# Optimization experiments

Measured on AMD Instinct MI355X. Metric: run time of the kernel, lower is better.

The kernel has to match this reference:

```python
import jax, jax.numpy as jnp
import numpy as np
import math

B, T, C, H = 2, 2048, 1024, 16
HD = C // H

def setup_inputs() -> dict:
    key = jax.random.key(0)
    ks = jax.random.split(key, 5)
    s_in = 1.0 / math.sqrt(C)
    x = jax.random.normal(ks[0], (B, T, C), dtype=jnp.float32)
    W_attn = jax.random.normal(ks[1], (C, 3 * C), dtype=jnp.float32) * s_in
    b_attn = jnp.zeros((3 * C,), dtype=jnp.float32)
    W_proj = jax.random.normal(ks[2], (C, C), dtype=jnp.float32) * s_in
    b_proj = jnp.zeros((C,), dtype=jnp.float32)
    return {"x": x, "W_attn": W_attn, "b_attn": b_attn, "W_proj": W_proj, "b_proj": b_proj}

def reference(x, W_attn, b_attn, W_proj, b_proj):
    Bx, Tx, Cx = x.shape
    c = x @ W_attn + b_attn  # [B,T,3C]
    q, k, v = jnp.split(c, 3, axis=2)
    # [B,T,H,hd] -> [B,H,T,hd]
    q = q.reshape(Bx, Tx, H, HD).transpose(0, 2, 1, 3)
    k = k.reshape(Bx, Tx, H, HD).transpose(0, 2, 1, 3)
    v = v.reshape(Bx, Tx, H, HD).transpose(0, 2, 1, 3)
    # NOTE: module scales by 1/sqrt(C), not 1/sqrt(head_dim)
    attn = jnp.einsum('bhqd,bhkd->bhqk', q, k) * (1.0 / math.sqrt(Cx))
    causal = jnp.tril(jnp.ones((Tx, Tx), dtype=bool))
    attn = jnp.where(causal[None, None], attn, -jnp.inf)
    attn = jax.nn.softmax(attn, axis=-1)
    y = jnp.einsum('bhqk,bhkd->bhqd', attn, v)
    y = y.transpose(0, 2, 1, 3).reshape(Bx, Tx, Cx)
    return y @ W_proj + b_proj
```

## Files before the change

### kernel.cpp

```cpp
#include <hip/hip_runtime.h>
#include <math.h>

#define Bv 2
#define Tv 2048
#define Cv 1024
#define Hv 16
#define HDv 64
#define Mv (Bv * Tv)
#define SZv (Bv * Hv * Tv * HDv)

typedef short bf16x8 __attribute__((ext_vector_type(8)));
typedef float f32x4 __attribute__((ext_vector_type(4)));

static __device__ __forceinline__ unsigned short f2bf(float f) {
    unsigned u = __float_as_uint(f);
    u += 0x7fffu + ((u >> 16) & 1u);
    return (unsigned short)(u >> 16);
}

static __device__ __forceinline__ unsigned f2bf2(float a, float b) {
    unsigned r;
    asm("v_cvt_pk_bf16_f32 %0, %1, %2" : "=v"(r) : "v"(a), "v"(b));
    return r;
}

#define AS1 __attribute__((address_space(1)))
#define AS3 __attribute__((address_space(3)))
#define GLD16(gp, lp) __builtin_amdgcn_global_load_lds( \
    (AS1 const void*)(const void*)(gp), (AS3 void*)(void*)(lp), 16, 0, 0)

#define WAITVM(n) asm volatile("s_waitcnt vmcnt(" #n ")" ::: "memory")
#define WAITLGKM0 asm volatile("s_waitcnt lgkmcnt(0)" ::: "memory")
#define BARRIER   asm volatile("s_barrier" ::: "memory")

__global__ __launch_bounds__(256) void prep_kernel(
    const float* __restrict__ x, const float* __restrict__ Wa,
    const float* __restrict__ Wp,
    unsigned short* __restrict__ xB, unsigned short* __restrict__ WaT,
    unsigned short* __restrict__ WpT)
{
    __shared__ float tile[32][33];
    const int bid = blockIdx.x;
    const int tid = threadIdx.x;

    if (bid < 4096) {
        int i = bid * 256 + tid;
        float4 f = ((const float4*)x)[i];
        ushort4 u;
        u.x = f2bf(f.x); u.y = f2bf(f.y); u.z = f2bf(f.z); u.w = f2bf(f.w);
        ((ushort4*)xB)[i] = u;
        return;
    }
    const float* src; unsigned short* dst; int Ncols, bi;
    if (bid < 7168) { bi = bid - 4096; Ncols = 3072; src = Wa; dst = WaT; }
    else            { bi = bid - 7168; Ncols = 1024; src = Wp; dst = WpT; }
    const int nct = Ncols / 32;
    const int c0 = (bi % nct) * 32, r0 = (bi / nct) * 32;
    const int tx = tid & 31, ty = tid >> 5;
    #pragma unroll
    for (int i = 0; i < 4; ++i)
        tile[ty + i * 8][tx] = src[(size_t)(r0 + ty + i * 8) * Ncols + c0 + tx];
    __syncthreads();
    #pragma unroll
    for (int i = 0; i < 4; ++i)
        dst[(size_t)(c0 + ty + i * 8) * Cv + r0 + tx] = f2bf(tile[tx][ty + i * 8]);
}

template<int AG>
__device__ __forceinline__ void mm_mainloop_1024(
    const unsigned short* __restrict__ A, const unsigned short* __restrict__ Bt,
    unsigned short* lds, int rowBase, int colBase, f32x4 acc[][4])
{
    const int tid  = threadIdx.x;
    const int lane = tid & 63;
    const int w    = tid >> 6;
    const int quad = lane >> 4, l15 = lane & 15;
    const int wm = (w >> 1) * (32 * AG), wn = (w & 1) * 64;
    const int K = 1024;
    constexpr int ASZ = 2048 * AG;
    constexpr int BUF = ASZ + 4096;
    constexpr int MI  = 2 * AG;

    size_t offA[AG]; unsigned short* ldsA[AG];
    size_t offB[2];  unsigned short* ldsB[2];
    #pragma unroll
    for (int i = 0; i < AG; ++i) {
        int g = w * (64 * AG) + i * 64 + lane;
        int r = g >> 2, kc = (g & 3) ^ ((r >> 1) & 3);
        offA[i] = (size_t)(rowBase + r) * K + kc * 8;
        ldsA[i] = lds + (w * AG + i) * 512;
    }
    #pragma unroll
    for (int i = 0; i < 2; ++i) {
        int g = w * 128 + i * 64 + lane;
        int r = g >> 2, kc = (g & 3) ^ ((r >> 1) & 3);
        offB[i] = (size_t)(colBase + r) * K + kc * 8;
        ldsB[i] = lds + ASZ + (w * 2 + i) * 512;
    }

    const int sw = quad ^ ((l15 >> 1) & 3);
    int aoff[MI], boff[4];
    #pragma unroll
    for (int i = 0; i < MI; ++i) aoff[i] = ((wm + i * 16 + l15) * 4 + sw) * 8;
    #pragma unroll
    for (int i = 0; i < 4; ++i)  boff[i] = ASZ + ((wn + i * 16 + l15) * 4 + sw) * 8;

    #pragma unroll
    for (int t = 0; t < 2; ++t) {
        #pragma unroll
        for (int i = 0; i < AG; ++i) GLD16(A + offA[i] + t * 32, ldsA[i] + t * BUF);
        #pragma unroll
        for (int i = 0; i < 2; ++i)  GLD16(Bt + offB[i] + t * 32, ldsB[i] + t * BUF);
    }

    int cur = 0;
    for (int i = 0; i < 32; ++i) {
        if (i < 31) {
            if constexpr (AG == 2) { WAITVM(4); } else { WAITVM(3); }
        } else { WAITVM(0); }
        BARRIER;
        if (i < 30) {
            int nb = cur + 2 * BUF; if (nb >= 3 * BUF) nb -= 3 * BUF;
            const int k2 = (i + 2) * 32;
            #pragma unroll
            for (int ai = 0; ai < AG; ++ai) GLD16(A + offA[ai] + k2, ldsA[ai] + nb);
            #pragma unroll
            for (int bi = 0; bi < 2; ++bi)  GLD16(Bt + offB[bi] + k2, ldsB[bi] + nb);
        }

        bf16x8 a[MI], b[4];
        #pragma unroll
        for (int j = 0; j < MI; ++j) a[j] = *(const bf16x8*)(lds + cur + aoff[j]);
        #pragma unroll
        for (int j = 0; j < 4; ++j)  b[j] = *(const bf16x8*)(lds + cur + boff[j]);

        #pragma unroll
        for (int mi = 0; mi < MI; ++mi)
            #pragma unroll
            for (int ni = 0; ni < 4; ++ni)
                acc[mi][ni] = __builtin_amdgcn_mfma_f32_16x16x32_bf16(
                    a[mi], b[ni], acc[mi][ni], 0, 0, 0);

        cur += BUF; if (cur == 3 * BUF) cur = 0;
    }
}

__global__ __launch_bounds__(256) void qkv_mm_kernel(
    const unsigned short* __restrict__ xB, const unsigned short* __restrict__ WaT,
    const float* __restrict__ bias,
    unsigned short* __restrict__ qB, unsigned short* __restrict__ kB,
    unsigned short* __restrict__ vT)
{
    __shared__ __align__(16) unsigned short lds[24576];
    const int rowBase = blockIdx.y * 128;
    const int colBase = blockIdx.x * 128;

    f32x4 acc[4][4];
    #pragma unroll
    for (int i = 0; i < 4; ++i)
        #pragma unroll
        for (int j = 0; j < 4; ++j) acc[i][j] = (f32x4){0.f, 0.f, 0.f, 0.f};

    mm_mainloop_1024<2>(xB, WaT, lds, rowBase, colBase, acc);
    __syncthreads();

    const int tid = threadIdx.x, lane = tid & 63, w = tid >> 6;
    const int quad = lane >> 4, l15 = lane & 15;
    const int wm = (w >> 1) * 64, wn = (w & 1) * 64;
    const int s = colBase / Cv;
    const int tloc = rowBase & (Tv - 1);
    const int bh0 = (rowBase / Tv) * Hv + (colBase % Cv) / HDv;

    if (s < 2) {
        const float qs = (s == 0) ? 0.04508422f : 1.0f;
        #pragma unroll
        for (int mi = 0; mi < 4; ++mi)
            #pragma unroll
            for (int ni = 0; ni < 4; ++ni) {
                float bv = bias[colBase + wn + ni * 16 + l15];
                #pragma unroll
                for (int r = 0; r < 4; ++r) {
                    int m = wm + mi * 16 + quad * 4 + r;
                    int n = wn + ni * 16 + l15;
                    lds[m * 136 + n] = f2bf((acc[mi][ni][r] + bv) * qs);
                }
            }
        __syncthreads();
        unsigned short* dst = (s == 0) ? qB : kB;
        #pragma unroll
        for (int it = 0; it < 8; ++it) {
            int cc = tid + it * 256;
            int m = cc >> 4, j = cc & 15;
            uint4 v = *(const uint4*)(lds + m * 136 + j * 8);
            int hh = j >> 3, d0 = (j & 7) * 8;
            *(uint4*)(dst + ((size_t)(bh0 + hh) * Tv + tloc + m) * HDv + d0) = v;
        }
    } else {
        #pragma unroll
        for (int mi = 0; mi < 4; ++mi)
            #pragma unroll
            for (int ni = 0; ni < 4; ++ni) {
                float bv = bias[colBase + wn + ni * 16 + l15];
                #pragma unroll
                for (int r = 0; r < 4; ++r) {
                    int m = wm + mi * 16 + quad * 4 + r;
                    int n = wn + ni * 16 + l15;
                    lds[n * 136 + m] = f2bf(acc[mi][ni][r] + bv);
                }
            }
        __syncthreads();
        #pragma unroll
        for (int it = 0; it < 8; ++it) {
            int cc = tid + it * 256;
            int n = cc >> 4, j = cc & 15;
            uint4 v = *(const uint4*)(lds + n * 136 + j * 8);
            int hh = n >> 6, d = n & 63;
            *(uint4*)(vT + ((size_t)(bh0 + hh) * HDv + d) * Tv + tloc + j * 8) = v;
        }
    }
}

__global__ __launch_bounds__(256) void proj_mm_kernel(
    const unsigned short* __restrict__ y0B, const unsigned short* __restrict__ WpT,
    const float* __restrict__ bias, float* __restrict__ out)
{
    __shared__ __align__(16) unsigned short lds[18432];
    const int rowBase = blockIdx.y * 64;
    const int colBase = blockIdx.x * 128;

    f32x4 acc[2][4];
    #pragma unroll
    for (int i = 0; i < 2; ++i)
        #pragma unroll
        for (int j = 0; j < 4; ++j) acc[i][j] = (f32x4){0.f, 0.f, 0.f, 0.f};

    mm_mainloop_1024<1>(y0B, WpT, lds, rowBase, colBase, acc);

    const int tid = threadIdx.x, lane = tid & 63, w = tid >> 6;
    const int quad = lane >> 4, l15 = lane & 15;
    const int wm = (w >> 1) * 32, wn = (w & 1) * 64;

    #pragma unroll
    for (int mi = 0; mi < 2; ++mi)
        #pragma unroll
        for (int ni = 0; ni < 4; ++ni) {
            int n = colBase + wn + ni * 16 + l15;
            float bv = bias[n];
            #pragma unroll
            for (int r = 0; r < 4; ++r) {
                int m = rowBase + wm + mi * 16 + quad * 4 + r;
                out[(size_t)m * Cv + n] = acc[mi][ni][r] + bv;
            }
        }
}

__global__ __launch_bounds__(256, 2) void attn_kernel(
    const unsigned short* __restrict__ qB, const unsigned short* __restrict__ kB,
    const unsigned short* __restrict__ vT, unsigned short* __restrict__ y0B)
{
    __shared__ __align__(16) unsigned short kv[2 * 8192];
    __shared__ __align__(16) unsigned short Pb[2][4][32 * 72];

    const int tid  = threadIdx.x;
    const int lane = tid & 63;
    const int w    = tid >> 6;
    const int quad = lane >> 4;
    const int l15  = lane & 15;

    const int j  = blockIdx.x >> 5;
    const int bh = blockIdx.x & 31;
    const int qA = j, qBt = 31 - j;
    const int tw = (w < 2) ? qA : qBt;
    const int ktmax = qBt;
    const int qwbase = tw * 64 + (w & 1) * 32;

    bf16x8 Qf[2][2];
    #pragma unroll
    for (int rg = 0; rg < 2; ++rg) {
        const unsigned short* qrow =
            qB + ((size_t)bh * Tv + qwbase + rg * 16 + l15) * HDv;
        Qf[rg][0] = *(const bf16x8*)(qrow + quad * 8);
        Qf[rg][1] = *(const bf16x8*)(qrow + 32 + quad * 8);
    }
    WAITVM(0);

    f32x4 O[2][4];
    float l[2][4];
    #pragma unroll
    for (int rg = 0; rg < 2; ++rg)
        #pragma unroll
        for (int n = 0; n < 4; ++n) {
            O[rg][n] = (f32x4){0.f, 0.f, 0.f, 0.f};
            l[rg][n] = 0.f;
        }

    const unsigned short* Kbase = kB + (size_t)bh * Tv * HDv;
    const unsigned short* Vbase = vT + (size_t)bh * HDv * Tv;
    unsigned short* Pw0 = &Pb[0][w][0];
    unsigned short* Pw1 = &Pb[1][w][0];

    const unsigned short* gK[2]; unsigned short* dK[2];
    const unsigned short* gV[2]; unsigned short* dV[2];
    #pragma unroll
    for (int i = 0; i < 2; ++i) {
        int slot = tid + i * 256;
        int row = slot >> 3;
        int gk = (slot & 7) ^ ((row >> 2) & 7);
        gK[i] = Kbase + row * HDv + gk * 8;
        dK[i] = kv + (size_t)(i * 256 + w * 64) * 8;
        int d = slot >> 3;
        int gv = (slot & 7) ^ (d & 7);
        gV[i] = Vbase + (size_t)d * Tv + gv * 8;
        dV[i] = kv + 4096 + (size_t)(i * 256 + w * 64) * 8;
    }

    int koff[4][2], voff[4][2];
    #pragma unroll
    for (int ct = 0; ct < 4; ++ct) {
        int row = ct + 4 * l15;
        #pragma unroll
        for (int jj = 0; jj < 2; ++jj)
            koff[ct][jj] = (row * 8 + ((quad + 4 * jj) ^ (l15 & 7))) * 8;
    }
    #pragma unroll
    for (int nt = 0; nt < 4; ++nt) {
        int d = nt * 16 + l15;
        #pragma unroll
        for (int jj = 0; jj < 2; ++jj)
            voff[nt][jj] = 4096 + (d * 8 + ((quad + 4 * jj) ^ (l15 & 7))) * 8;
    }

    GLD16(gK[0], dK[0]);
    GLD16(gK[1], dK[1]);
    GLD16(gV[0], dV[0]);
    GLD16(gV[1], dV[1]);

    bf16x8 Vprev[4][2];
    int cur = 0;
    for (int kt = 0; kt <= ktmax; ++kt) {
        WAITVM(0);
        BARRIER;
        if (kt < ktmax) {
            const int kb1 = (kt + 1) * 64;
            const int nxt = 8192 - cur;
            GLD16(gK[0] + (size_t)kb1 * HDv, dK[0] + nxt);
            GLD16(gK[1] + (size_t)kb1 * HDv, dK[1] + nxt);
            GLD16(gV[0] + kb1, dV[0] + nxt);
            GLD16(gV[1] + kb1, dV[1] + nxt);
        }

        unsigned short* PwW = (kt & 1) ? Pw1 : Pw0;
        unsigned short* PwR = (kt & 1) ? Pw0 : Pw1;

        if (kt > 0 && kt - 1 <= tw) {
            #pragma unroll
            for (int rg = 0; rg < 2; ++rg) {
                const bf16x8 Pa0 = *(const bf16x8*)(PwR + (rg * 16 + l15) * 72 + quad * 8);
                const bf16x8 Pa1 = *(const bf16x8*)(PwR + (rg * 16 + l15) * 72 + 32 + quad * 8);
                #pragma unroll
                for (int nt = 0; nt < 4; ++nt) {
                    O[rg][nt] = __builtin_amdgcn_mfma_f32_16x16x32_bf16(Pa0, Vprev[nt][0], O[rg][nt], 0, 0, 0);
                    O[rg][nt] = __builtin_amdgcn_mfma_f32_16x16x32_bf16(Pa1, Vprev[nt][1], O[rg][nt], 0, 0, 0);
                }
            }
        }

        if (kt <= tw) {
            bf16x8 Kb[4][2];
            #pragma unroll
            for (int ct = 0; ct < 4; ++ct) {
                Kb[ct][0] = *(const bf16x8*)(kv + cur + koff[ct][0]);
                Kb[ct][1] = *(const bf16x8*)(kv + cur + koff[ct][1]);
            }
            f32x4 S[2][4];
            #pragma unroll
            for (int rg = 0; rg < 2; ++rg)
                #pragma unroll
                for (int ct = 0; ct < 4; ++ct) {
                    S[rg][ct] = (f32x4){0.f, 0.f, 0.f, 0.f};
                    S[rg][ct] = __builtin_amdgcn_mfma_f32_16x16x32_bf16(Qf[rg][0], Kb[ct][0], S[rg][ct], 0, 0, 0);
                    S[rg][ct] = __builtin_amdgcn_mfma_f32_16x16x32_bf16(Qf[rg][1], Kb[ct][1], S[rg][ct], 0, 0, 0);
                }

            #pragma unroll
            for (int nt = 0; nt < 4; ++nt) {
                Vprev[nt][0] = *(const bf16x8*)(kv + cur + voff[nt][0]);
                Vprev[nt][1] = *(const bf16x8*)(kv + cur + voff[nt][1]);
            }

            if (kt == tw) {
                const int qloc = (w & 1) * 32;
                #pragma unroll
                for (int rg = 0; rg < 2; ++rg)
                    #pragma unroll
                    for (int ct = 0; ct < 4; ++ct)
                        #pragma unroll
                        for (int r = 0; r < 4; ++r)
                            if (ct + 4 * l15 > qloc + rg * 16 + quad * 4 + r)
                                S[rg][ct][r] = -1e30f;
            }

            #pragma unroll
            for (int rg = 0; rg < 2; ++rg) {
                float p[4][4];
                #pragma unroll
                for (int ct = 0; ct < 4; ++ct)
                    #pragma unroll
                    for (int r = 0; r < 4; ++r)
                        p[ct][r] = __builtin_amdgcn_exp2f(S[rg][ct][r]);
                #pragma unroll
                for (int r = 0; r < 4; ++r)
                    l[rg][r] += (p[0][r] + p[1][r]) + (p[2][r] + p[3][r]);

                #pragma unroll
                for (int r = 0; r < 4; ++r) {
                    uint2 u = make_uint2(f2bf2(p[0][r], p[1][r]), f2bf2(p[2][r], p[3][r]));
                    *(uint2*)(PwW + (rg * 16 + quad * 4 + r) * 72 + l15 * 4) = u;
                }
            }
        }

        cur = 8192 - cur;
    }

    if (tw == ktmax) {
        unsigned short* PwR = (ktmax & 1) ? Pw1 : Pw0;
        #pragma unroll
        for (int rg = 0; rg < 2; ++rg) {
            const bf16x8 Pa0 = *(const bf16x8*)(PwR + (rg * 16 + l15) * 72 + quad * 8);
            const bf16x8 Pa1 = *(const bf16x8*)(PwR + (rg * 16 + l15) * 72 + 32 + quad * 8);
            #pragma unroll
            for (int nt = 0; nt < 4; ++nt) {
                O[rg][nt] = __builtin_amdgcn_mfma_f32_16x16x32_bf16(Pa0, Vprev[nt][0], O[rg][nt], 0, 0, 0);
                O[rg][nt] = __builtin_amdgcn_mfma_f32_16x16x32_bf16(Pa1, Vprev[nt][1], O[rg][nt], 0, 0, 0);
            }
        }
    }

    #pragma unroll
    for (int rg = 0; rg < 2; ++rg)
        #pragma unroll
        for (int r = 0; r < 4; ++r) {
            l[rg][r] += __shfl_xor(l[rg][r], 1);
            l[rg][r] += __shfl_xor(l[rg][r], 2);
            l[rg][r] += __shfl_xor(l[rg][r], 4);
            l[rg][r] += __shfl_xor(l[rg][r], 8);
        }

    const int b = bh >> 4, h = bh & 15;
    #pragma unroll
    for (int rg = 0; rg < 2; ++rg)
        #pragma unroll
        for (int r = 0; r < 4; ++r) {
            float inv = 1.f / l[rg][r];
            int q = qwbase + rg * 16 + quad * 4 + r;
            unsigned short* dst = y0B + ((size_t)(b * Tv + q)) * Cv + h * HDv + l15;
            #pragma unroll
            for (int n = 0; n < 4; ++n) dst[n * 16] = f2bf(O[rg][n][r] * inv);
        }
}

extern "C" void kernel_launch(void* const* d_in, const int* in_sizes, int n_in,
                              void* d_out, int out_size, void* d_ws, size_t ws_size,
                              hipStream_t stream) {
    const float* x      = (const float*)d_in[0];
    const float* W_attn = (const float*)d_in[1];
    const float* b_attn = (const float*)d_in[2];
    const float* W_proj = (const float*)d_in[3];
    const float* b_proj = (const float*)d_in[4];
    float* out = (float*)d_out;

    unsigned short* xB  = (unsigned short*)d_ws;
    unsigned short* WaT = xB  + (size_t)Mv * Cv;
    unsigned short* WpT = WaT + (size_t)3 * Cv * Cv;
    unsigned short* qB  = WpT + (size_t)Cv * Cv;
    unsigned short* kB  = qB + (size_t)SZv;
    unsigned short* vT  = kB + (size_t)SZv;
    unsigned short* y0B = vT + (size_t)SZv;

    dim3 blk(256);
    prep_kernel<<<dim3(8192), blk, 0, stream>>>(x, W_attn, W_proj, xB, WaT, WpT);
    qkv_mm_kernel<<<dim3(3 * Cv / 128, Mv / 128), blk, 0, stream>>>(xB, WaT, b_attn, qB, kB, vT);
    attn_kernel<<<dim3(32 * 16), blk, 0, stream>>>(qB, kB, vT, y0B);
    proj_mm_kernel<<<dim3(Cv / 128, Mv / 64), blk, 0, stream>>>(y0B, WpT, b_proj, out);
}
```

Before: 173.5 us.

## Keep P in registers via transposed S=K·Q MFMA and triple-buffer K/V loads

The attention kernel computes S transposed (K as the A operand, Q as B), so the exp'd probabilities land in a register layout that feeds the PV MFMA directly. This removes the per-wave LDS round trip for P and the deferred Vprev pipeline. K/V tiles are now triple-buffered with two tiles prefetched ahead, and occupancy is raised to 3 blocks/CU. The work split changes from paired light/heavy q-tiles to one 128-row q tile per block, scheduled heaviest first, and the QKV epilogue permutes rows to match the new K layout. The cost is losing the paired load balancing, plus extra shuffles to gather the row sums.

```diff
diff --git a/kernel.cpp b/kernel.cpp
--- a/kernel.cpp
+++ b/kernel.cpp
@@ -30,7 +30,6 @@
     (AS1 const void*)(const void*)(gp), (AS3 void*)(void*)(lp), 16, 0, 0)
 
 #define WAITVM(n) asm volatile("s_waitcnt vmcnt(" #n ")" ::: "memory")
-#define WAITLGKM0 asm volatile("s_waitcnt lgkmcnt(0)" ::: "memory")
 #define BARRIER   asm volatile("s_barrier" ::: "memory")
 
 __global__ __launch_bounds__(256) void prep_kernel(
@@ -204,8 +203,11 @@
                 #pragma unroll
                 for (int r = 0; r < 4; ++r) {
                     int m = wm + mi * 16 + quad * 4 + r;
+                    int mk = m & 31;
+                    int mp = (m & ~31) | (mk & 3) | (((mk >> 4) & 1) << 2)
+                           | (((mk >> 2) & 3) << 3);
                     int n = wn + ni * 16 + l15;
-                    lds[n * 136 + m] = f2bf(acc[mi][ni][r] + bv);
+                    lds[n * 136 + mp] = f2bf(acc[mi][ni][r] + bv);
                 }
             }
         __syncthreads();
@@ -254,12 +256,11 @@
         }
 }
 
-__global__ __launch_bounds__(256, 2) void attn_kernel(
+__global__ __launch_bounds__(256, 3) void attn_kernel(
     const unsigned short* __restrict__ qB, const unsigned short* __restrict__ kB,
     const unsigned short* __restrict__ vT, unsigned short* __restrict__ y0B)
 {
-    __shared__ __align__(16) unsigned short kv[2 * 8192];
-    __shared__ __align__(16) unsigned short Pb[2][4][32 * 72];
+    __shared__ __align__(16) unsigned short kv[3 * 8192];
 
     const int tid  = threadIdx.x;
     const int lane = tid & 63;
@@ -267,37 +268,31 @@
     const int quad = lane >> 4;
     const int l15  = lane & 15;
 
-    const int j  = blockIdx.x >> 5;
+    const int qt = 15 - (blockIdx.x >> 5);
     const int bh = blockIdx.x & 31;
-    const int qA = j, qBt = 31 - j;
-    const int tw = (w < 2) ? qA : qBt;
-    const int ktmax = qBt;
-    const int qwbase = tw * 64 + (w & 1) * 32;
+    const int ktmax = 2 * qt + 1;
+    const int ktw   = 2 * qt + (w >> 1);
+    const int qbase = qt * 128 + w * 32;
 
     bf16x8 Qf[2][2];
     #pragma unroll
     for (int rg = 0; rg < 2; ++rg) {
         const unsigned short* qrow =
-            qB + ((size_t)bh * Tv + qwbase + rg * 16 + l15) * HDv;
+            qB + ((size_t)bh * Tv + qbase + rg * 16 + l15) * HDv;
         Qf[rg][0] = *(const bf16x8*)(qrow + quad * 8);
         Qf[rg][1] = *(const bf16x8*)(qrow + 32 + quad * 8);
     }
     WAITVM(0);
 
     f32x4 O[2][4];
-    float l[2][4];
+    float l[2] = {0.f, 0.f};
     #pragma unroll
     for (int rg = 0; rg < 2; ++rg)
         #pragma unroll
-        for (int n = 0; n < 4; ++n) {
-            O[rg][n] = (f32x4){0.f, 0.f, 0.f, 0.f};
-            l[rg][n] = 0.f;
-        }
+        for (int n = 0; n < 4; ++n) O[rg][n] = (f32x4){0.f, 0.f, 0.f, 0.f};
 
     const unsigned short* Kbase = kB + (size_t)bh * Tv * HDv;
     const unsigned short* Vbase = vT + (size_t)bh * HDv * Tv;
-    unsigned short* Pw0 = &Pb[0][w][0];
-    unsigned short* Pw1 = &Pb[1][w][0];
 
     const unsigned short* gK[2]; unsigned short* dK[2];
     const unsigned short* gV[2]; unsigned short* dV[2];
@@ -305,7 +300,7 @@
     for (int i = 0; i < 2; ++i) {
         int slot = tid + i * 256;
         int row = slot >> 3;
-        int gk = (slot & 7) ^ ((row >> 2) & 7);
+        int gk = (slot & 7) ^ (row & 7);
         gK[i] = Kbase + row * HDv + gk * 8;
         dK[i] = kv + (size_t)(i * 256 + w * 64) * 8;
         int d = slot >> 3;
@@ -316,147 +311,122 @@
 
     int koff[4][2], voff[4][2];
     #pragma unroll
-    for (int ct = 0; ct < 4; ++ct) {
-        int row = ct + 4 * l15;
+    for (int ct = 0; ct < 4; ++ct)
         #pragma unroll
         for (int jj = 0; jj < 2; ++jj)
-            koff[ct][jj] = (row * 8 + ((quad + 4 * jj) ^ (l15 & 7))) * 8;
-    }
-    #pragma unroll
-    for (int nt = 0; nt < 4; ++nt) {
-        int d = nt * 16 + l15;
-        #pragma unroll
-        for (int jj = 0; jj < 2; ++jj)
-            voff[nt][jj] = 4096 + (d * 8 + ((quad + 4 * jj) ^ (l15 & 7))) * 8;
-    }
-
-    GLD16(gK[0], dK[0]);
-    GLD16(gK[1], dK[1]);
-    GLD16(gV[0], dV[0]);
-    GLD16(gV[1], dV[1]);
-
-    bf16x8 Vprev[4][2];
+            koff[ct][jj] = ((ct * 16 + l15) * 8 + ((jj * 4 + quad) ^ (l15 & 7))) * 8;
+    #pragma unroll
+    for (int nt = 0; nt < 4; ++nt)
+        #pragma unroll
+        for (int hh = 0; hh < 2; ++hh)
+            voff[nt][hh] = 4096 + ((nt * 16 + l15) * 8 + ((quad + 4 * hh) ^ (l15 & 7))) * 8;
+
+#define STAGE(t, bufoff) do { \
+    GLD16(gK[0] + (size_t)(t) * 64 * HDv, dK[0] + (bufoff)); \
+    GLD16(gK[1] + (size_t)(t) * 64 * HDv, dK[1] + (bufoff)); \
+    GLD16(gV[0] + (t) * 64, dV[0] + (bufoff)); \
+    GLD16(gV[1] + (t) * 64, dV[1] + (bufoff)); \
+} while (0)
+
+    STAGE(0, 0);
+    STAGE(1, 8192);
+
     int cur = 0;
     for (int kt = 0; kt <= ktmax; ++kt) {
-        WAITVM(0);
+        if (kt < ktmax) { WAITVM(4); } else { WAITVM(0); }
         BARRIER;
-        if (kt < ktmax) {
-            const int kb1 = (kt + 1) * 64;
-            const int nxt = 8192 - cur;
-            GLD16(gK[0] + (size_t)kb1 * HDv, dK[0] + nxt);
-            GLD16(gK[1] + (size_t)kb1 * HDv, dK[1] + nxt);
-            GLD16(gV[0] + kb1, dV[0] + nxt);
-            GLD16(gV[1] + kb1, dV[1] + nxt);
-        }
-
-        unsigned short* PwW = (kt & 1) ? Pw1 : Pw0;
-        unsigned short* PwR = (kt & 1) ? Pw0 : Pw1;
-
-        if (kt > 0 && kt - 1 <= tw) {
-            #pragma unroll
-            for (int rg = 0; rg < 2; ++rg) {
-                const bf16x8 Pa0 = *(const bf16x8*)(PwR + (rg * 16 + l15) * 72 + quad * 8);
-                const bf16x8 Pa1 = *(const bf16x8*)(PwR + (rg * 16 + l15) * 72 + 32 + quad * 8);
-                #pragma unroll
-                for (int nt = 0; nt < 4; ++nt) {
-                    O[rg][nt] = __builtin_amdgcn_mfma_f32_16x16x32_bf16(Pa0, Vprev[nt][0], O[rg][nt], 0, 0, 0);
-                    O[rg][nt] = __builtin_amdgcn_mfma_f32_16x16x32_bf16(Pa1, Vprev[nt][1], O[rg][nt], 0, 0, 0);
+        if (kt + 2 <= ktmax) {
+            int nb = cur + 16384; if (nb >= 24576) nb -= 24576;
+            STAGE(kt + 2, nb);
+        }
+
+        if (kt <= ktw) {
+            const unsigned short* kvc = kv + cur;
+            #pragma unroll
+            for (int hh = 0; hh < 2; ++hh) {
+                bf16x8 Kb[2][2];
+                #pragma unroll
+                for (int c2 = 0; c2 < 2; ++c2) {
+                    int ct = hh * 2 + c2;
+                    Kb[c2][0] = *(const bf16x8*)(kvc + koff[ct][0]);
+                    Kb[c2][1] = *(const bf16x8*)(kvc + koff[ct][1]);
+                }
+                bf16x8 Vb[4];
+                #pragma unroll
+                for (int nt = 0; nt < 4; ++nt)
+                    Vb[nt] = *(const bf16x8*)(kvc + voff[nt][hh]);
+
+                f32x4 S[2][2];
+                #pragma unroll
+                for (int rg = 0; rg < 2; ++rg)
+                    #pragma unroll
+                    for (int c2 = 0; c2 < 2; ++c2) {
+                        S[rg][c2] = (f32x4){0.f, 0.f, 0.f, 0.f};
+                        S[rg][c2] = __builtin_amdgcn_mfma_f32_16x16x32_bf16(
+                            Kb[c2][0], Qf[rg][0], S[rg][c2], 0, 0, 0);
+                        S[rg][c2] = __builtin_amdgcn_mfma_f32_16x16x32_bf16(
+                            Kb[c2][1], Qf[rg][1], S[rg][c2], 0, 0, 0);
+                    }
+
+                if (kt == ktw) {
+                    const int kb2 = (w >> 1) * 64 + hh * 32;
+                    #pragma unroll
+                    for (int rg = 0; rg < 2; ++rg) {
+                        const int rrel = w * 32 + rg * 16 + l15;
+                        #pragma unroll
+                        for (int c2 = 0; c2 < 2; ++c2)
+                            #pragma unroll
+                            for (int r = 0; r < 4; ++r)
+                                if (kb2 + c2 * 16 + quad * 4 + r > rrel)
+                                    S[rg][c2][r] = -1e30f;
+                    }
+                }
+
+                #pragma unroll
+                for (int rg = 0; rg < 2; ++rg) {
+                    float p0[4], p1[4];
+                    #pragma unroll
+                    for (int r = 0; r < 4; ++r) {
+                        p0[r] = __builtin_amdgcn_exp2f(S[rg][0][r]);
+                        p1[r] = __builtin_amdgcn_exp2f(S[rg][1][r]);
+                    }
+                    l[rg] += ((p0[0] + p0[1]) + (p0[2] + p0[3]))
+                           + ((p1[0] + p1[1]) + (p1[2] + p1[3]));
+
+                    union { unsigned u[4]; bf16x8 v; } pa;
+                    pa.u[0] = f2bf2(p0[0], p0[1]);
+                    pa.u[1] = f2bf2(p0[2], p0[3]);
+                    pa.u[2] = f2bf2(p1[0], p1[1]);
+                    pa.u[3] = f2bf2(p1[2], p1[3]);
+                    #pragma unroll
+                    for (int nt = 0; nt < 4; ++nt)
+                        O[rg][nt] = __builtin_amdgcn_mfma_f32_16x16x32_bf16(
+                            pa.v, Vb[nt], O[rg][nt], 0, 0, 0);
                 }
             }
         }
 
-        if (kt <= tw) {
-            bf16x8 Kb[4][2];
-            #pragma unroll
-            for (int ct = 0; ct < 4; ++ct) {
-                Kb[ct][0] = *(const bf16x8*)(kv + cur + koff[ct][0]);
-                Kb[ct][1] = *(const bf16x8*)(kv + cur + koff[ct][1]);
-            }
-            f32x4 S[2][4];
-            #pragma unroll
-            for (int rg = 0; rg < 2; ++rg)
-                #pragma unroll
-                for (int ct = 0; ct < 4; ++ct) {
-                    S[rg][ct] = (f32x4){0.f, 0.f, 0.f, 0.f};
-                    S[rg][ct] = __builtin_amdgcn_mfma_f32_16x16x32_bf16(Qf[rg][0], Kb[ct][0], S[rg][ct], 0, 0, 0);
-                    S[rg][ct] = __builtin_amdgcn_mfma_f32_16x16x32_bf16(Qf[rg][1], Kb[ct][1], S[rg][ct], 0, 0, 0);
-                }
-
-            #pragma unroll
-            for (int nt = 0; nt < 4; ++nt) {
-                Vprev[nt][0] = *(const bf16x8*)(kv + cur + voff[nt][0]);
-                Vprev[nt][1] = *(const bf16x8*)(kv + cur + voff[nt][1]);
-            }
-
-            if (kt == tw) {
-                const int qloc = (w & 1) * 32;
-                #pragma unroll
-                for (int rg = 0; rg < 2; ++rg)
-                    #pragma unroll
-                    for (int ct = 0; ct < 4; ++ct)
-                        #pragma unroll
-                        for (int r = 0; r < 4; ++r)
-                            if (ct + 4 * l15 > qloc + rg * 16 + quad * 4 + r)
-                                S[rg][ct][r] = -1e30f;
-            }
-
-            #pragma unroll
-            for (int rg = 0; rg < 2; ++rg) {
-                float p[4][4];
-                #pragma unroll
-                for (int ct = 0; ct < 4; ++ct)
-                    #pragma unroll
-                    for (int r = 0; r < 4; ++r)
-                        p[ct][r] = __builtin_amdgcn_exp2f(S[rg][ct][r]);
-                #pragma unroll
-                for (int r = 0; r < 4; ++r)
-                    l[rg][r] += (p[0][r] + p[1][r]) + (p[2][r] + p[3][r]);
-
-                #pragma unroll
-                for (int r = 0; r < 4; ++r) {
-                    uint2 u = make_uint2(f2bf2(p[0][r], p[1][r]), f2bf2(p[2][r], p[3][r]));
-                    *(uint2*)(PwW + (rg * 16 + quad * 4 + r) * 72 + l15 * 4) = u;
-                }
-            }
-        }
-
-        cur = 8192 - cur;
-    }
-
-    if (tw == ktmax) {
-        unsigned short* PwR = (ktmax & 1) ? Pw1 : Pw0;
-        #pragma unroll
-        for (int rg = 0; rg < 2; ++rg) {
-            const bf16x8 Pa0 = *(const bf16x8*)(PwR + (rg * 16 + l15) * 72 + quad * 8);
-            const bf16x8 Pa1 = *(const bf16x8*)(PwR + (rg * 16 + l15) * 72 + 32 + quad * 8);
-            #pragma unroll
-            for (int nt = 0; nt < 4; ++nt) {
-                O[rg][nt] = __builtin_amdgcn_mfma_f32_16x16x32_bf16(Pa0, Vprev[nt][0], O[rg][nt], 0, 0, 0);
-                O[rg][nt] = __builtin_amdgcn_mfma_f32_16x16x32_bf16(Pa1, Vprev[nt][1], O[rg][nt], 0, 0, 0);
-            }
-        }
-    }
-
+        cur += 8192; if (cur == 24576) cur = 0;
+    }
+#undef STAGE
+
+    #pragma unroll
+    for (int rg = 0; rg < 2; ++rg) {
+        l[rg] += __shfl_xor(l[rg], 16);
+        l[rg] += __shfl_xor(l[rg], 32);
+    }
+
+    const int b = bh >> 4, h = bh & 15;
     #pragma unroll
     for (int rg = 0; rg < 2; ++rg)
         #pragma unroll
         for (int r = 0; r < 4; ++r) {
-            l[rg][r] += __shfl_xor(l[rg][r], 1);
-            l[rg][r] += __shfl_xor(l[rg][r], 2);
-            l[rg][r] += __shfl_xor(l[rg][r], 4);
-            l[rg][r] += __shfl_xor(l[rg][r], 8);
-        }
-
-    const int b = bh >> 4, h = bh & 15;
-    #pragma unroll
-    for (int rg = 0; rg < 2; ++rg)
-        #pragma unroll
-        for (int r = 0; r < 4; ++r) {
-            float inv = 1.f / l[rg][r];
-            int q = qwbase + rg * 16 + quad * 4 + r;
+            float lr = __shfl(l[rg], quad * 4 + r);
+            float inv = 1.f / lr;
+            int q = qbase + rg * 16 + quad * 4 + r;
             unsigned short* dst = y0B + ((size_t)(b * Tv + q)) * Cv + h * HDv + l15;
             #pragma unroll
-            for (int n = 0; n < 4; ++n) dst[n * 16] = f2bf(O[rg][n][r] * inv);
+            for (int nt = 0; nt < 4; ++nt) dst[nt * 16] = f2bf(O[rg][nt][r] * inv);
         }
 }
 
```

Measured after the change: 164.7 us. 5.1% less time.
